# Performance work log

Hardware: AMD Instinct MI355X
Metric: run time of the kernel (lower is better)

Reference implementation:

```python
import jax, jax.numpy as jnp
import numpy as np
from jax import lax

NUM_ANCHORS = 3
NUM_CLASSES = 80
SCORE_THRESH = 0.3
NMS_THRESH = 0.45
TOPK = 128  # max kept candidates per class per image (fixed-shape NMS)
REDUCTIONS = (8, 16, 32)
_ANCHORS = np.array([[12, 16], [19, 36], [40, 28], [36, 75], [76, 55], [72, 146],
                     [142, 110], [192, 243], [459, 401]], dtype=np.float32).reshape(3, 3, 2)


def _decode(pred, anchors):
    # pred: [b, A*(5+C), h, w]; anchors: [A,2] already divided by reduction
    b, c, h, w = pred.shape
    p = pred.reshape(b, NUM_ANCHORS, 5 + NUM_CLASSES, h * w).transpose(0, 1, 3, 2)  # [b,A,hw,5+C]
    gx = (jnp.arange(h * w) % w).astype(p.dtype)   # grid x offset per flattened cell
    gy = (jnp.arange(h * w) // w).astype(p.dtype)  # grid y offset
    cx = (jax.nn.sigmoid(p[..., 0]) + gx) / w
    cy = (jax.nn.sigmoid(p[..., 1]) + gy) / h
    bw = jnp.exp(p[..., 2]) * (anchors[:, 0] / w)[None, :, None]
    bh = jnp.exp(p[..., 3]) * (anchors[:, 1] / h)[None, :, None]
    x1 = cx - 0.5 * bw
    y1 = cy - 0.5 * bh
    boxes = jnp.stack([x1, y1, x1 + bw, y1 + bh], axis=-1)  # [b,A,hw,4] xyxy, normalized
    scores = jax.nn.sigmoid(p[..., 4])[..., None] * jax.nn.sigmoid(p[..., 5:])  # [b,A,hw,C]
    return boxes, scores


def _nms_single(boxes, probs):
    # boxes: [N,4]; probs: [N] with below-threshold entries masked to -1.
    # Greedy NMS on top-K candidates sorted by score (same math as the numpy loop).
    vals, idx = lax.top_k(probs, TOPK)
    bx = boxes[idx]                                            # [K,4] sorted by score desc
    area = (bx[:, 2] - bx[:, 0]) * (bx[:, 3] - bx[:, 1])
    tl = jnp.maximum(bx[:, None, :2], bx[None, :, :2])
    br = jnp.minimum(bx[:, None, 2:], bx[None, :, 2:])
    whi = jnp.clip(br - tl, 0.0)
    inter = whi[..., 0] * whi[..., 1]
    iou = inter / (area[:, None] + area[None, :] - inter)      # [K,K]
    ar = jnp.arange(TOPK)

    def step(p, i):
        sup = (iou[i] > NMS_THRESH) & (ar > i) & (p[i] > 0)
        return jnp.where(sup, -1.0, p), None

    p, _ = lax.scan(step, vals, ar)
    keep = p > 0
    return jnp.where(keep[:, None], bx, 0.0), jnp.where(keep, p, 0.0)


def reference(preds0, preds1, preds2):
    boxes_list, score_list = [], []
    for pred, red, anc in zip((preds0, preds1, preds2), REDUCTIONS, _ANCHORS):
        bx, sc = _decode(pred, jnp.asarray(anc) / red)
        boxes_list.append(bx)
        score_list.append(sc)
    boxes = jnp.concatenate(boxes_list, axis=2)
    scores = jnp.concatenate(score_list, axis=2)
    b = boxes.shape[0]
    boxes = boxes.reshape(b, -1, 4)              # [b, N, 4],  N = A * sum(hw)
    scores = scores.reshape(b, -1, NUM_CLASSES)  # [b, N, C]
    probs = jnp.where(scores > SCORE_THRESH, scores, -1.0)
    per_class = jax.vmap(_nms_single, in_axes=(None, 1))        # map over classes
    out_boxes, out_scores = jax.vmap(per_class)(boxes, probs)   # [b,C,K,4], [b,C,K]
    cls_id = jnp.broadcast_to(
        jnp.arange(NUM_CLASSES, dtype=out_boxes.dtype)[None, :, None], out_scores.shape)
    # [b, C, K, 6] = (x1, y1, x2, y2, score, class_id); zeroed rows = no detection
    return jnp.concatenate([out_boxes, out_scores[..., None], cls_id[..., None]], axis=-1)


def setup_inputs():
    key = jax.random.key(0)
    k0, k1, k2 = jax.random.split(key, 3)
    C = NUM_ANCHORS * (5 + NUM_CLASSES)
    return {
        "preds0": jax.random.normal(k0, (16, C, 76, 76), jnp.float32),
        "preds1": jax.random.normal(k1, (16, C, 38, 38), jnp.float32),
        "preds2": jax.random.normal(k2, (16, C, 19, 19), jnp.float32),
    }
```

## Files before the change

### kernel.cpp

```cpp
#include <hip/hip_runtime.h>
#include <math.h>
#include <stdint.h>

#define BATCH 16
#define NCLS 80
#define SUMHW 7581
#define NN 22743
#define ASTRIDE 7584
#define PADNN (3 * ASTRIDE)
#define TOPK 128
#define CAP 1024
#define WCAP 512
#define PRUNECAP 512
#define KEYBASE 0x3E800000u
#define KB2     0x3F180000u
#define SBITS   0x3F19999Au

typedef float f32x4 __attribute__((ext_vector_type(4)));

__device__ __forceinline__ float sigf(float x) {
    float e = (float)exp(-(double)x);
    return 1.0f / (1.0f + e);
}
__device__ __forceinline__ float expf_cr(float x) {
    return (float)exp((double)x);
}

struct DecParams { float aw[9]; float ah[9]; };

__global__ __launch_bounds__(256) void decode_kernel(
        const float* __restrict__ p0, const float* __restrict__ p1,
        const float* __restrict__ p2,
        float* __restrict__ so_arr, float* __restrict__ xthr_arr) {
    int blk = blockIdx.x;
    int b = blk / 27;
    int rem = blk % 27;
    int a = rem / 9;
    int seg = rem % 9;
    int s, segi;
    if (seg < 6)      { s = 0; segi = seg; }
    else if (seg < 8) { s = 1; segi = seg - 6; }
    else              { s = 2; segi = 0; }
    const int HW_[3]  = {5776, 1444, 361};
    const int OFF_[3] = {0, 5776, 7220};
    const float* __restrict__ pr = (s == 0) ? p0 : (s == 1) ? p1 : p2;
    int HW = HW_[s], OFF = OFF_[s];
    int t = threadIdx.x;

    auto mkthr = [](float so) {
        float thr = __int_as_float(0x7F800000);
        if (so > 0.59999f) {
            double arg = (double)so / 0.59999 - 1.0;
            thr = __double2float_rd(-log(arg));
        }
        return thr;
    };

    if (s != 2) {
        int cell0 = segi * 1024 + t * 4;
        if (cell0 >= HW) return;
        const float4* ob4 =
            (const float4*)(pr + ((size_t)b * 255 + (size_t)a * 85 + 4) * (size_t)HW);
        float4 ov = ob4[cell0 >> 2];
        float4 sov, thv;
        sov.x = sigf(ov.x); thv.x = mkthr(sov.x);
        sov.y = sigf(ov.y); thv.y = mkthr(sov.y);
        sov.z = sigf(ov.z); thv.z = mkthr(sov.z);
        sov.w = sigf(ov.w); thv.w = mkthr(sov.w);
        size_t pidx = (size_t)b * PADNN + a * ASTRIDE + OFF + cell0;
        *(float4*)(so_arr + pidx)   = sov;
        *(float4*)(xthr_arr + pidx) = thv;
    } else {
        const float* ob = pr + ((size_t)b * 255 + (size_t)a * 85 + 4) * 361;
        for (int i = t; i < 361; i += 256) {
            float so = sigf(ob[i]);
            size_t pidx = (size_t)b * PADNN + a * ASTRIDE + 7220 + i;
            so_arr[pidx] = so;
            xthr_arr[pidx] = mkthr(so);
        }
    }
}

__global__ __launch_bounds__(256) void select_nms_kernel(
        const float* __restrict__ p0, const float* __restrict__ p1,
        const float* __restrict__ p2,
        const float* __restrict__ so_arr,
        const float* __restrict__ xthr_arr,
        DecParams dp,
        float* __restrict__ out) {
    __shared__ __attribute__((aligned(16))) unsigned char smem[24576];
    unsigned int* wn        = (unsigned int*)smem;
    unsigned long long* skey = (unsigned long long*)smem;
    unsigned int* kbuf      = (unsigned int*)(smem + 8192);
    unsigned int* nbuf      = (unsigned int*)(smem + 16384);
    unsigned long long* sorted = (unsigned long long*)(smem + 8192);
    unsigned long long* mskp   = (unsigned long long*)(smem + 9216);
    float4* bxs4            = (float4*)(smem + 16384);
    float*  pvs             = (float*)(smem + 18432);
    __shared__ unsigned int hist[512];
    __shared__ unsigned int sums[256];
    __shared__ unsigned int wvc[4];
    __shared__ unsigned long long aliveLDS[2];
    __shared__ unsigned int sh_bin, sh_above, gcount;

    int t = threadIdx.x;
    int w = t >> 6, lane = t & 63;
    int bid = blockIdx.x;
    int b = bid / NCLS;
    int c = bid % NCLS;

    if (t < 4) wvc[t] = 0;
    __syncthreads();

#pragma unroll
    for (int s = 0; s < 2; ++s) {
        const float* __restrict__ pr = (s == 0) ? p0 : p1;
        const int HW  = (s == 0) ? 5776 : 1444;
        const int OFF = (s == 0) ? 0 : 5776;
        const int nq  = HW >> 2;
        unsigned long long bx0 = (unsigned long long)(uintptr_t)
            (pr + ((size_t)b * 255 + 0 * 85 + 5 + (size_t)c) * (size_t)HW);
        unsigned long long bx1 = (unsigned long long)(uintptr_t)
            (pr + ((size_t)b * 255 + 1 * 85 + 5 + (size_t)c) * (size_t)HW);
        unsigned long long bx2 = (unsigned long long)(uintptr_t)
            (pr + ((size_t)b * 255 + 2 * 85 + 5 + (size_t)c) * (size_t)HW);
        unsigned long long bq0 = (unsigned long long)(uintptr_t)
            (xthr_arr + (size_t)b * PADNN + 0 * ASTRIDE + OFF);
        unsigned long long bq1 = (unsigned long long)(uintptr_t)
            (xthr_arr + (size_t)b * PADNN + 1 * ASTRIDE + OFF);
        unsigned long long bq2 = (unsigned long long)(uintptr_t)
            (xthr_arr + (size_t)b * PADNN + 2 * ASTRIDE + OFF);
        for (int i = t; i < nq; i += 256) {
            unsigned voff = (unsigned)i << 4;
            f32x4 x0, x1, x2, q0, q1, q2;
            asm volatile(
                "global_load_dwordx4 %0, %6, %7\n\t"
                "global_load_dwordx4 %1, %6, %8\n\t"
                "global_load_dwordx4 %2, %6, %9\n\t"
                "global_load_dwordx4 %3, %6, %10\n\t"
                "global_load_dwordx4 %4, %6, %11\n\t"
                "global_load_dwordx4 %5, %6, %12\n\t"
                "s_waitcnt vmcnt(0)"
                : "=&v"(x0), "=&v"(x1), "=&v"(x2),
                  "=&v"(q0), "=&v"(q1), "=&v"(q2)
                : "v"(voff), "s"(bx0), "s"(bx1), "s"(bx2),
                  "s"(bq0), "s"(bq1), "s"(bq2));
            unsigned m = 0;
            m |= (x0.x > q0.x) ? 0x001u : 0u;  m |= (x0.y > q0.y) ? 0x002u : 0u;
            m |= (x0.z > q0.z) ? 0x004u : 0u;  m |= (x0.w > q0.w) ? 0x008u : 0u;
            m |= (x1.x > q1.x) ? 0x010u : 0u;  m |= (x1.y > q1.y) ? 0x020u : 0u;
            m |= (x1.z > q1.z) ? 0x040u : 0u;  m |= (x1.w > q1.w) ? 0x080u : 0u;
            m |= (x2.x > q2.x) ? 0x100u : 0u;  m |= (x2.y > q2.y) ? 0x200u : 0u;
            m |= (x2.z > q2.z) ? 0x400u : 0u;  m |= (x2.w > q2.w) ? 0x800u : 0u;
            if (m) {
                int cellb = OFF + 4 * i;
                do {
                    int k = __ffs(m) - 1;
                    m &= m - 1;
                    int a = k >> 2, j = k & 3;
                    unsigned pos = atomicAdd(&wvc[w], 1u);
                    if (pos < WCAP) wn[w * WCAP + pos] =
                        (unsigned)(a * SUMHW + cellb + j);
                } while (m);
            }
        }
    }
#pragma unroll
    for (int a = 0; a < 3; ++a) {
        const float* __restrict__ cp =
            p2 + ((size_t)b * 255 + (size_t)a * 85 + 5 + (size_t)c) * 361;
        const float* __restrict__ xt = xthr_arr + (size_t)b * PADNN + a * ASTRIDE + 7220;
        int n0 = a * SUMHW + 7220;
        for (int i = t; i < 361; i += 256) {
            if (cp[i] > xt[i]) {
                unsigned pos = atomicAdd(&wvc[w], 1u);
                if (pos < WCAP) wn[w * WCAP + pos] = (unsigned)(n0 + i);
            }
        }
    }
    __syncthreads();

    unsigned cw0 = wvc[0], cw1 = wvc[1], cw2 = wvc[2], cw3 = wvc[3];
    bool ovf = (cw0 > WCAP) || (cw1 > WCAP) || (cw2 > WCAP) || (cw3 > WCAP);
    unsigned G = cw0 + cw1 + cw2 + cw3;
    bool fb = ovf || (G < TOPK);

    auto rankSelect = [&](unsigned Gc) {
        if (t < TOPK) sorted[t] = 0ULL;
        __syncthreads();
        unsigned i0 = t, i1 = t + 256, i2 = t + 512, i3 = t + 768;
        bool v0 = i0 < Gc, v1 = i1 < Gc, v2 = i2 < Gc, v3 = i3 < Gc;
        unsigned long long o0 = v0 ? skey[i0] : 0ULL;
        unsigned long long o1 = v1 ? skey[i1] : 0ULL;
        unsigned long long o2 = v2 ? skey[i2] : 0ULL;
        unsigned long long o3 = v3 ? skey[i3] : 0ULL;
        unsigned r0 = 0, r1 = 0, r2 = 0, r3 = 0;
        for (unsigned j = 0; j < Gc; ++j) {
            unsigned long long kj = skey[j];
            r0 += (kj > o0); r1 += (kj > o1); r2 += (kj > o2); r3 += (kj > o3);
        }
        if (v0 && r0 < TOPK) sorted[r0] = o0;
        if (v1 && r1 < TOPK) sorted[r1] = o1;
        if (v2 && r2 < TOPK) sorted[r2] = o2;
        if (v3 && r3 < TOPK) sorted[r3] = o3;
        __syncthreads();
    };

    if (!fb) {
        unsigned woff = 0;
        if (w > 0) woff += cw0;
        if (w > 1) woff += cw1;
        if (w > 2) woff += cw2;
        unsigned mycnt = (w == 0) ? cw0 : (w == 1) ? cw1 : (w == 2) ? cw2 : cw3;
        for (unsigned i = lane; i < mycnt; i += 64) {
            unsigned n = wn[w * WCAP + i];
            unsigned a = n / SUMHW;
            unsigned r = n - a * SUMHW;
            size_t cb = (size_t)b * 255 + (size_t)a * 85 + 5 + (size_t)c;
            float x;
            if (r < 5776u)      x = p0[cb * 5776 + r];
            else if (r < 7220u) x = p1[cb * 1444 + (r - 5776u)];
            else                x = p2[cb * 361  + (r - 7220u)];
            float so = so_arr[(size_t)b * PADNN + a * ASTRIDE + r];
            float st = 1.0f / (1.0f + __expf(-x));
            kbuf[woff + i] = __float_as_uint(st * so);
            nbuf[woff + i] = n;
        }
        for (int i = t; i < 512; i += 256) hist[i] = 0;
        if (t == 0) gcount = 0;
        __syncthreads();

        for (unsigned i = t; i < G; i += 256) {
            unsigned bin = (kbuf[i] - KB2) >> 14;
            if (bin > 511u) bin = 511u;
            atomicAdd(&hist[bin], 1u);
        }
        __syncthreads();
        unsigned m0 = hist[2 * t], m1 = hist[2 * t + 1];
        sums[t] = m0 + m1;
        __syncthreads();
        for (int d = 1; d < 256; d <<= 1) {
            unsigned v = sums[t];
            if (t + d < 256) v += sums[t + d];
            __syncthreads();
            sums[t] = v;
            __syncthreads();
        }
        unsigned si = sums[t], se = si - (m0 + m1);
        if (se < TOPK && TOPK <= si) {
            if (TOPK <= se + m1) { sh_bin = 2 * t + 1; sh_above = se; }
            else                 { sh_bin = 2 * t;     sh_above = se + m1; }
        }
        __syncthreads();
        unsigned B1 = sh_bin, above1 = sh_above;
        unsigned cntB = hist[B1];
        unsigned binlo = KB2 + (B1 << 14);
        if (above1 + cntB > PRUNECAP - 64) {
            fb = true;
        } else {
            unsigned gth = binlo - 256;
            for (unsigned i = t; i < G; i += 256) {
                if (kbuf[i] >= gth) {
                    unsigned pos = atomicAdd(&gcount, 1u);
                    if (pos < PRUNECAP) {
                        unsigned n = nbuf[i];
                        unsigned a = n / SUMHW;
                        unsigned r = n - a * SUMHW;
                        size_t cb = (size_t)b * 255 + (size_t)a * 85 + 5 + (size_t)c;
                        float x;
                        if (r < 5776u)      x = p0[cb * 5776 + r];
                        else if (r < 7220u) x = p1[cb * 1444 + (r - 5776u)];
                        else                x = p2[cb * 361  + (r - 7220u)];
                        float so = so_arr[(size_t)b * PADNN + a * ASTRIDE + r];
                        float ex = so * sigf(x);
                        skey[pos] = (ex > 0.3f)
                            ? (((unsigned long long)__float_as_uint(ex) << 32) |
                               (unsigned)(~n))
                            : (unsigned long long)(unsigned)(~n);
                    }
                }
            }
            __syncthreads();
            if (gcount > PRUNECAP) fb = true;
            if (!fb) {
                unsigned Gc = gcount;
                rankSelect(Gc);
                bool ok = (Gc >= TOPK) && ((unsigned)(sorted[TOPK - 1] >> 32) >= SBITS);
                if (!ok) fb = true;
            }
        }
    }

    if (fb) {
        auto scanScalar = [&](auto&& body) {
#pragma unroll
            for (int s = 0; s < 3; ++s) {
                const float* __restrict__ pr = (s == 0) ? p0 : (s == 1) ? p1 : p2;
                const int HW  = (s == 0) ? 5776 : (s == 1) ? 1444 : 361;
                const int OFF = (s == 0) ? 0 : (s == 1) ? 5776 : 7220;
#pragma unroll
                for (int a = 0; a < 3; ++a) {
                    const float* __restrict__ cp =
                        pr + ((size_t)b * 255 + (size_t)a * 85 + 5 + (size_t)c) * (size_t)HW;
                    const float* __restrict__ sop =
                        so_arr + (size_t)b * PADNN + a * ASTRIDE + OFF;
                    int n0 = a * SUMHW + OFF;
                    for (int i = t; i < HW; i += 256) {
                        float so = sop[i];
                        if (so <= 0.2999f) continue;
                        float x = cp[i];
                        float st = 1.0f / (1.0f + __expf(-x));
                        float sca = st * so;
                        if (sca > 0.2999f) body(sca, x, so, n0 + i);
                    }
                }
            }
        };
        __syncthreads();
        for (int i = t; i < 512; i += 256) hist[i] = 0;
        if (t == 0) gcount = 0;
        __syncthreads();
        scanScalar([&](float sca, float, float, int) {
            unsigned bin = (__float_as_uint(sca) - KEYBASE) >> 15;
            if (bin > 511u) bin = 511u;
            atomicAdd(&hist[bin], 1u);
        });
        __syncthreads();
        unsigned m0 = hist[2 * t], m1 = hist[2 * t + 1];
        sums[t] = m0 + m1;
        __syncthreads();
        for (int d = 1; d < 256; d <<= 1) {
            unsigned v = sums[t];
            if (t + d < 256) v += sums[t + d];
            __syncthreads();
            sums[t] = v;
            __syncthreads();
        }
        unsigned total = sums[0];
        bool gatherAll = (total < TOPK);
        unsigned gth = 0;
        if (!gatherAll) {
            unsigned si = sums[t], se = si - (m0 + m1);
            if (se < TOPK && TOPK <= si) {
                if (TOPK <= se + m1) { sh_bin = 2 * t + 1; sh_above = se; }
                else                 { sh_bin = 2 * t;     sh_above = se + m1; }
            }
            __syncthreads();
            unsigned B1 = sh_bin, above1 = sh_above;
            unsigned cntB = hist[B1];
            unsigned binlo = KEYBASE + (B1 << 15);
            __syncthreads();
            if (above1 + cntB <= 768) {
                gth = binlo - 256;
            } else {
                if (t < 256) hist[t] = 0;
                __syncthreads();
                scanScalar([&](float sca, float, float, int) {
                    unsigned key = __float_as_uint(sca);
                    if (((key - KEYBASE) >> 15) == B1) {
                        unsigned sub = (key - binlo) >> 7;
                        if (sub > 255u) sub = 255u;
                        atomicAdd(&hist[sub], 1u);
                    }
                });
                __syncthreads();
                unsigned R2 = TOPK - above1;
                unsigned sl = hist[t];
                sums[t] = sl;
                __syncthreads();
                for (int d = 1; d < 256; d <<= 1) {
                    unsigned v = sums[t];
                    if (t + d < 256) v += sums[t + d];
                    __syncthreads();
                    sums[t] = v;
                    __syncthreads();
                }
                unsigned si2 = sums[t], se2 = si2 - sl;
                if (se2 < R2 && R2 <= si2) sh_bin = (unsigned)t;
                __syncthreads();
                gth = binlo + (sh_bin << 7) - 256;
            }
        }
        __syncthreads();
        scanScalar([&](float sca, float x, float so, int n) {
            unsigned key = __float_as_uint(sca);
            if (gatherAll || key >= gth) {
                unsigned pos = atomicAdd(&gcount, 1u);
                if (pos < CAP) {
                    float ex = so * sigf(x);
                    skey[pos] = (ex > 0.3f)
                        ? (((unsigned long long)__float_as_uint(ex) << 32) |
                           (unsigned)(~(unsigned)n))
                        : (unsigned long long)(unsigned)(~(unsigned)n);
                }
            }
        });
        __syncthreads();
        unsigned Gc = gcount < CAP ? gcount : CAP;
        rankSelect(Gc);
    }

    if (t < TOPK) {
        unsigned long long e = sorted[t];
        bool vld = (e != 0ULL);
        float sc = __uint_as_float((unsigned)(e >> 32));
        unsigned n = ~(unsigned)(e & 0xFFFFFFFFu);
        float4 bb = make_float4(0.f, 0.f, 0.f, 0.f);
        if (vld) {
            unsigned a = n / SUMHW;
            unsigned r = n - a * SUMHW;
            int s, S, HW, off; const float* pr;
            if (r < 5776u)      { s = 0; S = 76; HW = 5776; off = 0;    pr = p0; }
            else if (r < 7220u) { s = 1; S = 38; HW = 1444; off = 5776; pr = p1; }
            else                { s = 2; S = 19; HW = 361;  off = 7220; pr = p2; }
            int cell = (int)r - off;
            const float* pb = pr + ((size_t)b * 255 + (size_t)a * 85) * (size_t)HW + cell;
            float tx = pb[0];
            float ty = pb[(size_t)HW];
            float tw = pb[(size_t)2 * HW];
            float th = pb[(size_t)3 * HW];
            float Sf = (float)S;
            float gx = (float)(cell % S);
            float gy = (float)(cell / S);
            float cx = (sigf(tx) + gx) / Sf;
            float cy = (sigf(ty) + gy) / Sf;
            float aw = dp.aw[s * 3 + a], ah = dp.ah[s * 3 + a];
            float bw = expf_cr(tw) * aw;
            float bh = expf_cr(th) * ah;
            float x1 = cx - 0.5f * bw;
            float y1 = cy - 0.5f * bh;
            bb = make_float4(x1, y1, x1 + bw, y1 + bh);
        }
        bxs4[t] = bb;
        pvs[t] = vld ? sc : -1.0f;
    }
    __syncthreads();

    {
        int i = t >> 1, h = t & 1;
        float4 bi = bxs4[i];
        float ai = (bi.z - bi.x) * (bi.w - bi.y);
        unsigned long long m = 0;
        int jb = h << 6;
        for (int k = 0; k < 64; ++k) {
            int j = jb + k;
            float4 bj = bxs4[j];
            float aj = (bj.z - bj.x) * (bj.w - bj.y);
            float xx1 = fmaxf(bi.x, bj.x), yy1 = fmaxf(bi.y, bj.y);
            float xx2 = fminf(bi.z, bj.z), yy2 = fminf(bi.w, bj.w);
            float ww = fmaxf(xx2 - xx1, 0.0f), hh = fmaxf(yy2 - yy1, 0.0f);
            float inter = ww * hh;
            float iou = inter / (ai + aj - inter);
            if (j > i && iou > 0.45f) m |= (1ull << k);
        }
        mskp[(i << 1) | h] = m;
    }
    __syncthreads();
    if (t < 64) {
        unsigned long long A0 = __ballot(pvs[t] > 0.0f);
        unsigned long long A1 = __ballot(pvs[t + 64] > 0.0f);
        for (int i = 0; i < 64; ++i) {
            if ((A0 >> i) & 1) { A0 &= ~mskp[i << 1]; A1 &= ~mskp[(i << 1) | 1]; }
        }
        for (int i = 0; i < 64; ++i) {
            if ((A1 >> i) & 1) { A1 &= ~mskp[((64 + i) << 1) | 1]; }
        }
        if (t == 0) { aliveLDS[0] = A0; aliveLDS[1] = A1; }
    }
    __syncthreads();

    unsigned long long A0 = aliveLDS[0], A1 = aliveLDS[1];
    float* o = out + (size_t)bid * TOPK * 6;
    for (int i = t; i < TOPK; i += 256) {
        bool alive = (i < 64) ? ((A0 >> i) & 1) : ((A1 >> (i - 64)) & 1);
        float p = pvs[i];
        bool kept = alive && (p > 0.0f);
        float4 bb = bxs4[i];
        o[i * 6 + 0] = kept ? bb.x : 0.0f;
        o[i * 6 + 1] = kept ? bb.y : 0.0f;
        o[i * 6 + 2] = kept ? bb.z : 0.0f;
        o[i * 6 + 3] = kept ? bb.w : 0.0f;
        o[i * 6 + 4] = kept ? p : 0.0f;
        o[i * 6 + 5] = (float)c;
    }
}

extern "C" void kernel_launch(void* const* d_in, const int* in_sizes, int n_in,
                              void* d_out, int out_size, void* d_ws, size_t ws_size,
                              hipStream_t stream) {
    const float* p0 = (const float*)d_in[0];
    const float* p1 = (const float*)d_in[1];
    const float* p2 = (const float*)d_in[2];
    float* out = (float*)d_out;

    char* ws = (char*)d_ws;
    float* so_arr = (float*)ws;
    float* xthr   = (float*)(ws + 1456128ull);

    static const float ANC[3][3][2] = {
        {{12, 16}, {19, 36}, {40, 28}},
        {{36, 75}, {76, 55}, {72, 146}},
        {{142, 110}, {192, 243}, {459, 401}},
    };
    static const int RED[3] = {8, 16, 32};
    static const int SS[3]  = {76, 38, 19};

    DecParams dp;
    for (int s = 0; s < 3; ++s)
        for (int a = 0; a < 3; ++a) {
            float Sf = (float)SS[s];
            dp.aw[s * 3 + a] = (ANC[s][a][0] / (float)RED[s]) / Sf;
            dp.ah[s * 3 + a] = (ANC[s][a][1] / (float)RED[s]) / Sf;
        }

    decode_kernel<<<BATCH * 27, 256, 0, stream>>>(p0, p1, p2, so_arr, xthr);
    select_nms_kernel<<<BATCH * NCLS, 256, 0, stream>>>(p0, p1, p2, so_arr, xthr, dp, out);
}
```

Before: 74.00 us.

## Software-pipeline class-score loads in the select scan and shrink LDS for occupancy

The per-class threshold scan over the two larger scales now double-buffers its loads. The next iteration's class-logit loads are issued together with the current iteration's threshold loads, and a partial vmcnt wait lets compare-and-push overlap the outstanding memory traffic. Separately, the per-wave candidate capacity is cut from 512 to 384 and the shared buffer offsets are shrunk, with launch bounds asking for 8 blocks per CU, to raise occupancy. The trade-off is more frequent per-wave overflow into the slower fallback path, plus fragile inline-asm register dependencies across separate asm statements.

```diff
diff --git a/kernel.cpp b/kernel.cpp
--- a/kernel.cpp
+++ b/kernel.cpp
@@ -10,7 +10,8 @@
 #define PADNN (3 * ASTRIDE)
 #define TOPK 128
 #define CAP 1024
-#define WCAP 512
+#define WCAP 384
+#define GMAX (4 * WCAP)
 #define PRUNECAP 512
 #define KEYBASE 0x3E800000u
 #define KB2     0x3F180000u
@@ -81,22 +82,22 @@
     }
 }
 
-__global__ __launch_bounds__(256) void select_nms_kernel(
+__global__ __launch_bounds__(256, 8) void select_nms_kernel(
         const float* __restrict__ p0, const float* __restrict__ p1,
         const float* __restrict__ p2,
         const float* __restrict__ so_arr,
         const float* __restrict__ xthr_arr,
         DecParams dp,
         float* __restrict__ out) {
-    __shared__ __attribute__((aligned(16))) unsigned char smem[24576];
-    unsigned int* wn        = (unsigned int*)smem;
-    unsigned long long* skey = (unsigned long long*)smem;
-    unsigned int* kbuf      = (unsigned int*)(smem + 8192);
-    unsigned int* nbuf      = (unsigned int*)(smem + 16384);
-    unsigned long long* sorted = (unsigned long long*)(smem + 8192);
-    unsigned long long* mskp   = (unsigned long long*)(smem + 9216);
-    float4* bxs4            = (float4*)(smem + 16384);
-    float*  pvs             = (float*)(smem + 18432);
+    __shared__ __attribute__((aligned(16))) unsigned char smem[18432];
+    unsigned int* wn            = (unsigned int*)smem;
+    unsigned long long* skey    = (unsigned long long*)smem;
+    unsigned int* kbuf          = (unsigned int*)(smem + 6144);
+    unsigned int* nbuf          = (unsigned int*)(smem + 12288);
+    unsigned long long* sorted  = (unsigned long long*)(smem + 8192);
+    unsigned long long* mskp    = (unsigned long long*)(smem + 9216);
+    float4* bxs4                = (float4*)(smem + 12288);
+    float*  pvs                 = (float*)(smem + 14336);
     __shared__ unsigned int hist[512];
     __shared__ unsigned int sums[256];
     __shared__ unsigned int wvc[4];
@@ -112,12 +113,28 @@
     if (t < 4) wvc[t] = 0;
     __syncthreads();
 
-#pragma unroll
-    for (int s = 0; s < 2; ++s) {
-        const float* __restrict__ pr = (s == 0) ? p0 : p1;
-        const int HW  = (s == 0) ? 5776 : 1444;
-        const int OFF = (s == 0) ? 0 : 5776;
-        const int nq  = HW >> 2;
+    auto cmpPush = [&](f32x4 A0, f32x4 A1, f32x4 A2,
+                       f32x4 Q0, f32x4 Q1, f32x4 Q2, int cellb) {
+        unsigned m = 0;
+        m |= (A0.x > Q0.x) ? 0x001u : 0u;  m |= (A0.y > Q0.y) ? 0x002u : 0u;
+        m |= (A0.z > Q0.z) ? 0x004u : 0u;  m |= (A0.w > Q0.w) ? 0x008u : 0u;
+        m |= (A1.x > Q1.x) ? 0x010u : 0u;  m |= (A1.y > Q1.y) ? 0x020u : 0u;
+        m |= (A1.z > Q1.z) ? 0x040u : 0u;  m |= (A1.w > Q1.w) ? 0x080u : 0u;
+        m |= (A2.x > Q2.x) ? 0x100u : 0u;  m |= (A2.y > Q2.y) ? 0x200u : 0u;
+        m |= (A2.z > Q2.z) ? 0x400u : 0u;  m |= (A2.w > Q2.w) ? 0x800u : 0u;
+        if (m) {
+            do {
+                int k = __ffs(m) - 1;
+                m &= m - 1;
+                int a = k >> 2, j = k & 3;
+                unsigned pos = atomicAdd(&wvc[w], 1u);
+                if (pos < WCAP) wn[w * WCAP + pos] = (unsigned)(a * SUMHW + cellb + j);
+            } while (m);
+        }
+    };
+
+    auto scanPipe = [&](const float* __restrict__ pr, int HW, int OFF) {
+        const int nq = HW >> 2;
         unsigned long long bx0 = (unsigned long long)(uintptr_t)
             (pr + ((size_t)b * 255 + 0 * 85 + 5 + (size_t)c) * (size_t)HW);
         unsigned long long bx1 = (unsigned long long)(uintptr_t)
@@ -130,41 +147,61 @@
             (xthr_arr + (size_t)b * PADNN + 1 * ASTRIDE + OFF);
         unsigned long long bq2 = (unsigned long long)(uintptr_t)
             (xthr_arr + (size_t)b * PADNN + 2 * ASTRIDE + OFF);
-        for (int i = t; i < nq; i += 256) {
-            unsigned voff = (unsigned)i << 4;
-            f32x4 x0, x1, x2, q0, q1, q2;
-            asm volatile(
-                "global_load_dwordx4 %0, %6, %7\n\t"
-                "global_load_dwordx4 %1, %6, %8\n\t"
-                "global_load_dwordx4 %2, %6, %9\n\t"
-                "global_load_dwordx4 %3, %6, %10\n\t"
-                "global_load_dwordx4 %4, %6, %11\n\t"
-                "global_load_dwordx4 %5, %6, %12\n\t"
-                "s_waitcnt vmcnt(0)"
-                : "=&v"(x0), "=&v"(x1), "=&v"(x2),
-                  "=&v"(q0), "=&v"(q1), "=&v"(q2)
-                : "v"(voff), "s"(bx0), "s"(bx1), "s"(bx2),
-                  "s"(bq0), "s"(bq1), "s"(bq2));
-            unsigned m = 0;
-            m |= (x0.x > q0.x) ? 0x001u : 0u;  m |= (x0.y > q0.y) ? 0x002u : 0u;
-            m |= (x0.z > q0.z) ? 0x004u : 0u;  m |= (x0.w > q0.w) ? 0x008u : 0u;
-            m |= (x1.x > q1.x) ? 0x010u : 0u;  m |= (x1.y > q1.y) ? 0x020u : 0u;
-            m |= (x1.z > q1.z) ? 0x040u : 0u;  m |= (x1.w > q1.w) ? 0x080u : 0u;
-            m |= (x2.x > q2.x) ? 0x100u : 0u;  m |= (x2.y > q2.y) ? 0x200u : 0u;
-            m |= (x2.z > q2.z) ? 0x400u : 0u;  m |= (x2.w > q2.w) ? 0x800u : 0u;
-            if (m) {
-                int cellb = OFF + 4 * i;
-                do {
-                    int k = __ffs(m) - 1;
-                    m &= m - 1;
-                    int a = k >> 2, j = k & 3;
-                    unsigned pos = atomicAdd(&wvc[w], 1u);
-                    if (pos < WCAP) wn[w * WCAP + pos] =
-                        (unsigned)(a * SUMHW + cellb + j);
-                } while (m);
-            }
-        }
-    }
+        int i = t;
+        if (i >= nq) return;
+        f32x4 xa0, xa1, xa2, xb0, xb1, xb2, q0, q1, q2;
+        unsigned vo = (unsigned)i << 4;
+        asm volatile(
+            "global_load_dwordx4 %0, %3, %4\n\t"
+            "global_load_dwordx4 %1, %3, %5\n\t"
+            "global_load_dwordx4 %2, %3, %6"
+            : "=&v"(xa0), "=&v"(xa1), "=&v"(xa2)
+            : "v"(vo), "s"(bx0), "s"(bx1), "s"(bx2));
+        for (;;) {
+            {
+                int inext = i + 256;
+                bool last = inext >= nq;
+                unsigned von = (unsigned)(last ? i : inext) << 4;
+                asm volatile(
+                    "global_load_dwordx4 %0, %6, %7\n\t"
+                    "global_load_dwordx4 %1, %6, %8\n\t"
+                    "global_load_dwordx4 %2, %6, %9\n\t"
+                    "global_load_dwordx4 %3, %10, %11\n\t"
+                    "global_load_dwordx4 %4, %10, %12\n\t"
+                    "global_load_dwordx4 %5, %10, %13\n\t"
+                    "s_waitcnt vmcnt(3)"
+                    : "=&v"(q0), "=&v"(q1), "=&v"(q2),
+                      "=&v"(xb0), "=&v"(xb1), "=&v"(xb2)
+                    : "v"(vo), "s"(bq0), "s"(bq1), "s"(bq2),
+                      "v"(von), "s"(bx0), "s"(bx1), "s"(bx2));
+                cmpPush(xa0, xa1, xa2, q0, q1, q2, OFF + 4 * i);
+                if (last) { asm volatile("s_waitcnt vmcnt(0)"); break; }
+                i = inext; vo = von;
+            }
+            {
+                int inext = i + 256;
+                bool last = inext >= nq;
+                unsigned von = (unsigned)(last ? i : inext) << 4;
+                asm volatile(
+                    "global_load_dwordx4 %0, %6, %7\n\t"
+                    "global_load_dwordx4 %1, %6, %8\n\t"
+                    "global_load_dwordx4 %2, %6, %9\n\t"
+                    "global_load_dwordx4 %3, %10, %11\n\t"
+                    "global_load_dwordx4 %4, %10, %12\n\t"
+                    "global_load_dwordx4 %5, %10, %13\n\t"
+                    "s_waitcnt vmcnt(3)"
+                    : "=&v"(q0), "=&v"(q1), "=&v"(q2),
+                      "=&v"(xa0), "=&v"(xa1), "=&v"(xa2)
+                    : "v"(vo), "s"(bq0), "s"(bq1), "s"(bq2),
+                      "v"(von), "s"(bx0), "s"(bx1), "s"(bx2));
+                cmpPush(xb0, xb1, xb2, q0, q1, q2, OFF + 4 * i);
+                if (last) { asm volatile("s_waitcnt vmcnt(0)"); break; }
+                i = inext; vo = von;
+            }
+        }
+    };
+    scanPipe(p0, 5776, 0);
+    scanPipe(p1, 1444, 5776);
 #pragma unroll
     for (int a = 0; a < 3; ++a) {
         const float* __restrict__ cp =
```

New measurement: 74.14 us. About the same (+0.2%).

## Store raw logits with indices in LDS to avoid global re-reads

Applied to the files above, without the earlier changes.

During the threshold scan, each survivor's class logit is now stored next to its index as a 64-bit LDS entry. The later keying and pruning passes read the logit from there instead of reloading it from global memory through a branchy stage lookup. The histogram build is fused into the keying loop, which saves a pass and a barrier, and the single aliased shared buffer is split into dedicated arrays. Per-wave capacity drops from 512 to 320, so blocks with many survivors overflow into the slow fallback path more often, and LDS usage changes.

```diff
diff --git a/kernel.cpp b/kernel.cpp
--- a/kernel.cpp
+++ b/kernel.cpp
@@ -10,7 +10,8 @@
 #define PADNN (3 * ASTRIDE)
 #define TOPK 128
 #define CAP 1024
-#define WCAP 512
+#define WCAP 320
+#define GMAX (4 * WCAP)
 #define PRUNECAP 512
 #define KEYBASE 0x3E800000u
 #define KB2     0x3F180000u
@@ -88,15 +89,14 @@
         const float* __restrict__ xthr_arr,
         DecParams dp,
         float* __restrict__ out) {
-    __shared__ __attribute__((aligned(16))) unsigned char smem[24576];
-    unsigned int* wn        = (unsigned int*)smem;
-    unsigned long long* skey = (unsigned long long*)smem;
-    unsigned int* kbuf      = (unsigned int*)(smem + 8192);
-    unsigned int* nbuf      = (unsigned int*)(smem + 16384);
-    unsigned long long* sorted = (unsigned long long*)(smem + 8192);
-    unsigned long long* mskp   = (unsigned long long*)(smem + 9216);
-    float4* bxs4            = (float4*)(smem + 16384);
-    float*  pvs             = (float*)(smem + 18432);
+    __shared__ __attribute__((aligned(16))) unsigned long long wn64[4 * WCAP];
+    unsigned long long* skeyF = wn64;
+    __shared__ unsigned int kbuf[GMAX];
+    __shared__ unsigned long long skeyM[PRUNECAP];
+    __shared__ unsigned long long sorted[TOPK];
+    __shared__ unsigned long long mskp[2 * TOPK];
+    __shared__ float4 bxs4[TOPK];
+    __shared__ float pvs[TOPK];
     __shared__ unsigned int hist[512];
     __shared__ unsigned int sums[256];
     __shared__ unsigned int wvc[4];
@@ -110,14 +110,32 @@
     int c = bid % NCLS;
 
     if (t < 4) wvc[t] = 0;
+    for (int i = t; i < 512; i += 256) hist[i] = 0;
     __syncthreads();
 
-#pragma unroll
-    for (int s = 0; s < 2; ++s) {
-        const float* __restrict__ pr = (s == 0) ? p0 : p1;
-        const int HW  = (s == 0) ? 5776 : 1444;
-        const int OFF = (s == 0) ? 0 : 5776;
-        const int nq  = HW >> 2;
+    auto pushx = [&](float xv, int nn) {
+        unsigned pos = atomicAdd(&wvc[w], 1u);
+        if (pos < WCAP) wn64[w * WCAP + pos] =
+            ((unsigned long long)__float_as_uint(xv) << 32) | (unsigned)nn;
+    };
+    auto cmpPush = [&](f32x4 A0, f32x4 A1, f32x4 A2,
+                       f32x4 Q0, f32x4 Q1, f32x4 Q2, int cellb) {
+        if (A0.x > Q0.x) pushx(A0.x, cellb + 0);
+        if (A0.y > Q0.y) pushx(A0.y, cellb + 1);
+        if (A0.z > Q0.z) pushx(A0.z, cellb + 2);
+        if (A0.w > Q0.w) pushx(A0.w, cellb + 3);
+        if (A1.x > Q1.x) pushx(A1.x, SUMHW + cellb + 0);
+        if (A1.y > Q1.y) pushx(A1.y, SUMHW + cellb + 1);
+        if (A1.z > Q1.z) pushx(A1.z, SUMHW + cellb + 2);
+        if (A1.w > Q1.w) pushx(A1.w, SUMHW + cellb + 3);
+        if (A2.x > Q2.x) pushx(A2.x, 2 * SUMHW + cellb + 0);
+        if (A2.y > Q2.y) pushx(A2.y, 2 * SUMHW + cellb + 1);
+        if (A2.z > Q2.z) pushx(A2.z, 2 * SUMHW + cellb + 2);
+        if (A2.w > Q2.w) pushx(A2.w, 2 * SUMHW + cellb + 3);
+    };
+
+    auto scanBlock = [&](const float* __restrict__ pr, int HW, int OFF) {
+        const int nq = HW >> 2;
         unsigned long long bx0 = (unsigned long long)(uintptr_t)
             (pr + ((size_t)b * 255 + 0 * 85 + 5 + (size_t)c) * (size_t)HW);
         unsigned long long bx1 = (unsigned long long)(uintptr_t)
@@ -145,26 +163,11 @@
                   "=&v"(q0), "=&v"(q1), "=&v"(q2)
                 : "v"(voff), "s"(bx0), "s"(bx1), "s"(bx2),
                   "s"(bq0), "s"(bq1), "s"(bq2));
-            unsigned m = 0;
-            m |= (x0.x > q0.x) ? 0x001u : 0u;  m |= (x0.y > q0.y) ? 0x002u : 0u;
-            m |= (x0.z > q0.z) ? 0x004u : 0u;  m |= (x0.w > q0.w) ? 0x008u : 0u;
-            m |= (x1.x > q1.x) ? 0x010u : 0u;  m |= (x1.y > q1.y) ? 0x020u : 0u;
-            m |= (x1.z > q1.z) ? 0x040u : 0u;  m |= (x1.w > q1.w) ? 0x080u : 0u;
-            m |= (x2.x > q2.x) ? 0x100u : 0u;  m |= (x2.y > q2.y) ? 0x200u : 0u;
-            m |= (x2.z > q2.z) ? 0x400u : 0u;  m |= (x2.w > q2.w) ? 0x800u : 0u;
-            if (m) {
-                int cellb = OFF + 4 * i;
-                do {
-                    int k = __ffs(m) - 1;
-                    m &= m - 1;
-                    int a = k >> 2, j = k & 3;
-                    unsigned pos = atomicAdd(&wvc[w], 1u);
-                    if (pos < WCAP) wn[w * WCAP + pos] =
-                        (unsigned)(a * SUMHW + cellb + j);
-                } while (m);
-            }
-        }
-    }
+            cmpPush(x0, x1, x2, q0, q1, q2, OFF + 4 * i);
+        }
+    };
+    scanBlock(p0, 5776, 0);
+    scanBlock(p1, 1444, 5776);
 #pragma unroll
     for (int a = 0; a < 3; ++a) {
         const float* __restrict__ cp =
@@ -172,10 +175,8 @@
         const float* __restrict__ xt = xthr_arr + (size_t)b * PADNN + a * ASTRIDE + 7220;
         int n0 = a * SUMHW + 7220;
         for (int i = t; i < 361; i += 256) {
-            if (cp[i] > xt[i]) {
-                unsigned pos = atomicAdd(&wvc[w], 1u);
-                if (pos < WCAP) wn[w * WCAP + pos] = (unsigned)(n0 + i);
-            }
+            float xv = cp[i];
+            if (xv > xt[i]) pushx(xv, n0 + i);
         }
     }
     __syncthreads();
@@ -185,18 +186,18 @@
     unsigned G = cw0 + cw1 + cw2 + cw3;
     bool fb = ovf || (G < TOPK);
 
-    auto rankSelect = [&](unsigned Gc) {
+    auto rankSelect = [&](const unsigned long long* sk, unsigned Gc) {
         if (t < TOPK) sorted[t] = 0ULL;
         __syncthreads();
         unsigned i0 = t, i1 = t + 256, i2 = t + 512, i3 = t + 768;
         bool v0 = i0 < Gc, v1 = i1 < Gc, v2 = i2 < Gc, v3 = i3 < Gc;
-        unsigned long long o0 = v0 ? skey[i0] : 0ULL;
-        unsigned long long o1 = v1 ? skey[i1] : 0ULL;
-        unsigned long long o2 = v2 ? skey[i2] : 0ULL;
-        unsigned long long o3 = v3 ? skey[i3] : 0ULL;
+        unsigned long long o0 = v0 ? sk[i0] : 0ULL;
+        unsigned long long o1 = v1 ? sk[i1] : 0ULL;
+        unsigned long long o2 = v2 ? sk[i2] : 0ULL;
+        unsigned long long o3 = v3 ? sk[i3] : 0ULL;
         unsigned r0 = 0, r1 = 0, r2 = 0, r3 = 0;
         for (unsigned j = 0; j < Gc; ++j) {
-            unsigned long long kj = skey[j];
+            unsigned long long kj = sk[j];
             r0 += (kj > o0); r1 += (kj > o1); r2 += (kj > o2); r3 += (kj > o3);
         }
         if (v0 && r0 < TOPK) sorted[r0] = o0;
@@ -213,29 +214,22 @@
         if (w > 2) woff += cw2;
         unsigned mycnt = (w == 0) ? cw0 : (w == 1) ? cw1 : (w == 2) ? cw2 : cw3;
         for (unsigned i = lane; i < mycnt; i += 64) {
-            unsigned n = wn[w * WCAP + i];
+            unsigned long long e = wn64[w * WCAP + i];
+            float x = __uint_as_float((unsigned)(e >> 32));
+            unsigned n = (unsigned)(e & 0xFFFFFFFFu);
             unsigned a = n / SUMHW;
             unsigned r = n - a * SUMHW;
-            size_t cb = (size_t)b * 255 + (size_t)a * 85 + 5 + (size_t)c;
-            float x;
-            if (r < 5776u)      x = p0[cb * 5776 + r];
-            else if (r < 7220u) x = p1[cb * 1444 + (r - 5776u)];
-            else                x = p2[cb * 361  + (r - 7220u)];
             float so = so_arr[(size_t)b * PADNN + a * ASTRIDE + r];
             float st = 1.0f / (1.0f + __expf(-x));
-            kbuf[woff + i] = __float_as_uint(st * so);
-            nbuf[woff + i] = n;
-        }
-        for (int i = t; i < 512; i += 256) hist[i] = 0;
-        if (t == 0) gcount = 0;
-        __syncthreads();
-
-        for (unsigned i = t; i < G; i += 256) {
-            unsigned bin = (kbuf[i] - KB2) >> 14;
+            unsigned key = __float_as_uint(st * so);
+            kbuf[woff + i] = key;
+            unsigned bin = (key - KB2) >> 14;
             if (bin > 511u) bin = 511u;
             atomicAdd(&hist[bin], 1u);
         }
-        __syncthreads();
+        if (t == 0) gcount = 0;
+        __syncthreads();
+
         unsigned m0 = hist[2 * t], m1 = hist[2 * t + 1];
         sums[t] = m0 + m1;
         __syncthreads();
@@ -259,21 +253,24 @@
             fb = true;
         } else {
             unsigned gth = binlo - 256;
+            unsigned b1e = cw0, b2e = cw0 + cw1, b3e = b2e + cw2;
             for (unsigned i = t; i < G; i += 256) {
                 if (kbuf[i] >= gth) {
                     unsigned pos = atomicAdd(&gcount, 1u);
                     if (pos < PRUNECAP) {
-                        unsigned n = nbuf[i];
+                        unsigned w2, off2;
+                        if (i < b1e)      { w2 = 0; off2 = i; }
+                        else if (i < b2e) { w2 = 1; off2 = i - b1e; }
+                        else if (i < b3e) { w2 = 2; off2 = i - b2e; }
+                        else              { w2 = 3; off2 = i - b3e; }
+                        unsigned long long e = wn64[w2 * WCAP + off2];
+                        float x = __uint_as_float((unsigned)(e >> 32));
+                        unsigned n = (unsigned)(e & 0xFFFFFFFFu);
                         unsigned a = n / SUMHW;
                         unsigned r = n - a * SUMHW;
-                        size_t cb = (size_t)b * 255 + (size_t)a * 85 + 5 + (size_t)c;
-                        float x;
-                        if (r < 5776u)      x = p0[cb * 5776 + r];
-                        else if (r < 7220u) x = p1[cb * 1444 + (r - 5776u)];
-                        else                x = p2[cb * 361  + (r - 7220u)];
                         float so = so_arr[(size_t)b * PADNN + a * ASTRIDE + r];
                         float ex = so * sigf(x);
-                        skey[pos] = (ex > 0.3f)
+                        skeyM[pos] = (ex > 0.3f)
                             ? (((unsigned long long)__float_as_uint(ex) << 32) |
                                (unsigned)(~n))
                             : (unsigned long long)(unsigned)(~n);
@@ -284,7 +281,7 @@
             if (gcount > PRUNECAP) fb = true;
             if (!fb) {
                 unsigned Gc = gcount;
-                rankSelect(Gc);
+                rankSelect(skeyM, Gc);
                 bool ok = (Gc >= TOPK) && ((unsigned)(sorted[TOPK - 1] >> 32) >= SBITS);
                 if (!ok) fb = true;
             }
@@ -388,7 +385,7 @@
                 unsigned pos = atomicAdd(&gcount, 1u);
                 if (pos < CAP) {
                     float ex = so * sigf(x);
-                    skey[pos] = (ex > 0.3f)
+                    skeyF[pos] = (ex > 0.3f)
                         ? (((unsigned long long)__float_as_uint(ex) << 32) |
                            (unsigned)(~(unsigned)n))
                         : (unsigned long long)(unsigned)(~(unsigned)n);
@@ -397,7 +394,7 @@
         });
         __syncthreads();
         unsigned Gc = gcount < CAP ? gcount : CAP;
-        rankSelect(Gc);
+        rankSelect(skeyF, Gc);
     }
 
     if (t < TOPK) {
```

Result: faster. 68.44 us (-7.5%).
